# Kernel optimization log

Hardware: AMD Instinct MI355X
Metric: run time of the kernel (lower is better)

The kernel has to match this reference:

```python
import jax, jax.numpy as jnp
import numpy as np

N_NODES = 100000


def _gcn_conv(x, edge_index, W, b):
    """PyG GCNConv: add self-loops, symmetric deg^-1/2 normalization, scatter-add."""
    N = x.shape[0]
    h = x @ W  # [N, out]
    src = edge_index[0]
    dst = edge_index[1]
    loop = jnp.arange(N, dtype=src.dtype)
    src = jnp.concatenate([src, loop])
    dst = jnp.concatenate([dst, loop])
    deg = jax.ops.segment_sum(jnp.ones(src.shape[0], dtype=h.dtype), dst, num_segments=N)
    dinv = jnp.where(deg > 0, jax.lax.rsqrt(deg), 0.0)
    norm = dinv[src] * dinv[dst]  # [E+N]
    msgs = h[src] * norm[:, None]  # gather + scale
    out = jax.ops.segment_sum(msgs, dst, num_segments=N)  # scatter-add
    return out + b


def setup_inputs() -> dict:
    key = jax.random.key(0)
    k1, k2, k3, k4 = jax.random.split(key, 4)
    F_IN, H = 512, 16
    x = jax.random.normal(k1, (N_NODES, F_IN), dtype=jnp.float32)
    edge_index = jax.random.randint(k2, (2, 3200000), 0, N_NODES, dtype=jnp.int64)
    # Glorot init like PyG GCNConv
    lim = np.sqrt(6.0 / (F_IN + H)).astype(np.float32)
    W1 = jax.random.uniform(k3, (F_IN, H), dtype=jnp.float32, minval=-lim, maxval=lim)
    b1 = jnp.zeros((H,), dtype=jnp.float32)
    return {"x": x, "edge_index": edge_index, "W1": W1, "b1": b1}


def reference(x, edge_index, W1, b1):
    # forward: relu(GCNConv(x)); dropout is identity in eval; log_softmax over features
    h = jax.nn.relu(_gcn_conv(x, edge_index, W1, b1))
    return jax.nn.log_softmax(h, axis=1)
```

## Files before the change

### kernel.cpp

```cpp
#include <hip/hip_runtime.h>
#include <hip/hip_bf16.h>
#include <stdint.h>

#define N_NODES 100000
#define F_IN    512
#define HOUT    16

#define BSH   8
#define NBUK  391
#define CAP   9216
#define CHUNK 8192
#define GEMM_BLOCKS 782

typedef __attribute__((ext_vector_type(8))) short bf16x8;
typedef __attribute__((ext_vector_type(4))) float f32x4;

__device__ __forceinline__ short f2bf(float f) {
    union { float f; uint32_t u; } v; v.f = f;
    uint32_t r = (v.u + 0x7FFFu + ((v.u >> 16) & 1u)) >> 16;
    return (short)r;
}
__device__ __forceinline__ float bf2f(uint32_t bits16) {
    union { uint32_t u; float f; } v; v.u = bits16 << 16;
    return v.f;
}

__device__ __forceinline__ int edge_at(const void* ei, int64_t idx, uint32_t is64) {
    if (is64) return (int)((const long long*)ei)[idx];
    return ((const int*)ei)[idx];
}

__global__ void k_init(const uint32_t* __restrict__ e_u32, uint32_t* __restrict__ flag,
                       uint32_t* __restrict__ bucket_woff) {
    const int t = threadIdx.x;
    if (t < NBUK) bucket_woff[t] = 0u;
    if (t == 0) {
        uint32_t o = 0;
        #pragma unroll
        for (int i = 1; i < 32; i += 2) o |= e_u32[i];
        flag[0] = (o == 0u) ? 1u : 0u;
    }
}

__global__ __launch_bounds__(512) void k_fused(const void* __restrict__ ei, int E, int nchunks,
                                               const uint32_t* __restrict__ flag,
                                               uint32_t* __restrict__ bucket_woff,
                                               uint32_t* __restrict__ gpairs,
                                               const float* __restrict__ x,
                                               const float* __restrict__ W,
                                               ushort* __restrict__ hb) {
    __shared__ uint32_t h[512];
    __shared__ uint32_t ex[512];
    __shared__ uint32_t pcnt[512];
    __shared__ uint32_t gbase[512];
    __shared__ uint32_t sorted[CHUNK];
    __shared__ uint16_t sbuck[CHUNK];

    const int t = threadIdx.x;

    if ((int)blockIdx.x < nchunks) {
        const uint32_t is64 = flag[0];
        const int base = blockIdx.x * CHUNK;
        const int chunk_n = min(CHUNK, E - base);

        h[t] = 0;
        __syncthreads();

        uint32_t pr[16];
        uint16_t bk[16];
        #pragma unroll
        for (int k = 0; k < 16; ++k) {
            int e = base + k * 512 + t;
            bk[k] = 0xFFFFu;
            if (e < E) {
                uint32_t s = (uint32_t)edge_at(ei, e, is64);
                uint32_t d = (uint32_t)edge_at(ei, (int64_t)E + e, is64);
                uint32_t b = d >> BSH;
                pr[k] = (s << BSH) | (d & ((1u << BSH) - 1u));
                bk[k] = (uint16_t)b;
                atomicAdd(&h[b], 1u);
            }
        }
        __syncthreads();

        const uint32_t hv = h[t];
        for (int off = 1; off < 512; off <<= 1) {
            uint32_t v = (t >= off) ? h[t - off] : 0u;
            __syncthreads();
            h[t] += v;
            __syncthreads();
        }
        ex[t] = h[t] - hv;
        pcnt[t] = ex[t];
        if (t < NBUK) gbase[t] = atomicAdd(&bucket_woff[t], hv);
        __syncthreads();

        #pragma unroll
        for (int k = 0; k < 16; ++k) {
            if (bk[k] != 0xFFFFu) {
                uint32_t slot = atomicAdd(&pcnt[bk[k]], 1u);
                sorted[slot] = pr[k];
                sbuck[slot] = bk[k];
            }
        }
        __syncthreads();

        #pragma unroll
        for (int k = 0; k < 16; ++k) {
            int i = k * 512 + t;
            if (i < chunk_n) {
                uint32_t b = sbuck[i];
                uint32_t pos = gbase[b] + ((uint32_t)i - ex[b]);
                gpairs[(size_t)b * CAP + pos] = sorted[i];
            }
        }
    } else {
        const int lane = t & 63;
        const int wid  = t >> 6;
        const int tile = ((int)blockIdx.x - nchunks) * 8 + wid;
        if (tile * 16 >= N_NODES) return;
        const int c    = lane & 15;
        const int half = lane >> 4;

        bf16x8 bfrag[16];
        #pragma unroll
        for (int s = 0; s < 16; ++s) {
            #pragma unroll
            for (int e = 0; e < 8; ++e) {
                int k = 32 * s + 8 * half + e;
                bfrag[s][e] = f2bf(W[k * HOUT + c]);
            }
        }

        const int row = tile * 16 + c;
        const float* xr = x + (int64_t)row * F_IN;
        f32x4 acc = {0.f, 0.f, 0.f, 0.f};
        #pragma unroll
        for (int s = 0; s < 16; ++s) {
            const float4 a0 = *(const float4*)(xr + 32 * s + 8 * half);
            const float4 a1 = *(const float4*)(xr + 32 * s + 8 * half + 4);
            bf16x8 af;
            af[0] = f2bf(a0.x); af[1] = f2bf(a0.y); af[2] = f2bf(a0.z); af[3] = f2bf(a0.w);
            af[4] = f2bf(a1.x); af[5] = f2bf(a1.y); af[6] = f2bf(a1.z); af[7] = f2bf(a1.w);
            acc = __builtin_amdgcn_mfma_f32_16x16x32_bf16(af, bfrag[s], acc, 0, 0, 0);
        }

        #pragma unroll
        for (int r = 0; r < 4; ++r) {
            int orow = tile * 16 + 4 * half + r;
            hb[(int64_t)orow * HOUT + c] = (ushort)f2bf(acc[r]);
        }
    }
}

__global__ __launch_bounds__(256) void k_hist(const uint32_t* __restrict__ bucket_woff,
                                              const uint32_t* __restrict__ gpairs,
                                              uint32_t* __restrict__ cnt,
                                              ushort* __restrict__ hb) {
    const int b = blockIdx.x;
    const int t = threadIdx.x;
    const uint32_t count = bucket_woff[b];
    const uint32_t* gp = gpairs + (size_t)b * CAP;

    __shared__ uint32_t lc[256];
    lc[t] = 0;
    __syncthreads();
    for (uint32_t i = t; i < count; i += 256)
        atomicAdd(&lc[gp[i] & 255u], 1u);
    __syncthreads();

    const int gn = (b << BSH) + t;
    if (gn < N_NODES) {
        const uint32_t deg = lc[t];
        cnt[gn] = deg;
        const float dinv = rsqrtf((float)(deg + 1u));
        ushort* row = hb + (size_t)gn * HOUT;
        ulonglong4 rv = *(const ulonglong4*)row;
        ushort u[16];
        *(ulonglong4*)u = rv;
        #pragma unroll
        for (int q = 0; q < 16; ++q)
            u[q] = (ushort)f2bf(bf2f(u[q]) * dinv);
        *(ulonglong4*)row = *(const ulonglong4*)u;
    }
}

__global__ __launch_bounds__(1024) void k_sortagg(const uint32_t* __restrict__ bucket_woff,
                                                  const uint32_t* __restrict__ gpairs,
                                                  const uint32_t* __restrict__ cnt,
                                                  const ushort* __restrict__ hb,
                                                  const float* __restrict__ bias,
                                                  float* __restrict__ out) {
    const int bk = blockIdx.x;
    const int t = threadIdx.x;
    const uint32_t count = bucket_woff[bk];
    const uint32_t* gp = gpairs + (size_t)bk * CAP;

    __shared__ uint32_t lc[256];
    __shared__ uint32_t st[256];
    __shared__ uint32_t cur[256];
    __shared__ uint32_t sc[256];
    __shared__ uint32_t lsrc[CAP];

    if (t < 256) {
        int gn = (bk << BSH) + t;
        lc[t] = (gn < N_NODES) ? cnt[gn] : 0u;
        sc[t] = lc[t];
    }
    __syncthreads();
    for (int off = 1; off < 256; off <<= 1) {
        uint32_t v = 0;
        if (t < 256 && t >= off) v = sc[t - off];
        __syncthreads();
        if (t < 256) sc[t] += v;
        __syncthreads();
    }
    if (t < 256) {
        st[t] = sc[t] - lc[t];
        cur[t] = st[t];
    }
    __syncthreads();

    for (uint32_t i = t; i < count; i += 1024) {
        uint32_t p = gp[i];
        uint32_t pos = atomicAdd(&cur[p & 255u], 1u);
        lsrc[pos] = p >> BSH;
    }
    __syncthreads();

    const int f = t & 15;
    const int g = t >> 4;
    const float bf = bias[f];

    #pragma unroll
    for (int i = 0; i < 4; ++i) {
        int dl = g + 64 * i;
        int gn = (bk << BSH) + dl;
        if (gn >= N_NODES) break;
        const uint32_t s0 = st[dl];
        const uint32_t n  = lc[dl];

        float acc = 0.f;
        uint32_t j = 0;
        for (; j + 4 <= n; j += 4) {
            uint32_t a = lsrc[s0 + j], b2 = lsrc[s0 + j + 1];
            uint32_t c2 = lsrc[s0 + j + 2], d2 = lsrc[s0 + j + 3];
            float v0 = bf2f(hb[(size_t)a  * HOUT + f]);
            float v1 = bf2f(hb[(size_t)b2 * HOUT + f]);
            float v2 = bf2f(hb[(size_t)c2 * HOUT + f]);
            float v3 = bf2f(hb[(size_t)d2 * HOUT + f]);
            acc += (v0 + v1) + (v2 + v3);
        }
        for (; j < n; ++j)
            acc += bf2f(hb[(size_t)lsrc[s0 + j] * HOUT + f]);

        const float dinv = rsqrtf((float)(n + 1u));
        const float self = bf2f(hb[(size_t)gn * HOUT + f]);
        float v = fmaxf(fmaf(dinv, acc + self, bf), 0.f);

        float m = v;
        #pragma unroll
        for (int d = 1; d < 16; d <<= 1) m = fmaxf(m, __shfl_xor(m, d));
        float ex = __expf(v - m);
        float sum = ex;
        #pragma unroll
        for (int d = 1; d < 16; d <<= 1) sum += __shfl_xor(sum, d);
        out[(size_t)gn * HOUT + f] = v - (m + __logf(sum));
    }
}

extern "C" void kernel_launch(void* const* d_in, const int* in_sizes, int n_in,
                              void* d_out, int out_size, void* d_ws, size_t ws_size,
                              hipStream_t stream) {
    const float* x  = (const float*)d_in[0];
    const void*  ei = d_in[1];
    const float* W  = (const float*)d_in[2];
    const float* b  = (const float*)d_in[3];
    float* out = (float*)d_out;
    const int E = in_sizes[1] / 2;
    const int nchunks = (E + CHUNK - 1) / CHUNK;

    char* ws = (char*)d_ws;
    uint32_t* flag        = (uint32_t*)ws;
    uint32_t* bucket_woff = (uint32_t*)(ws + 1024);
    uint32_t* gpairs      = (uint32_t*)(ws + (1 << 20));
    ushort*   hb          = (ushort*)(ws + (16 << 20));
    uint32_t* cnt         = (uint32_t*)(ws + (20 << 20));

    k_init<<<1, 512, 0, stream>>>((const uint32_t*)ei, flag, bucket_woff);
    k_fused<<<nchunks + GEMM_BLOCKS, 512, 0, stream>>>(ei, E, nchunks, flag,
                                                       bucket_woff, gpairs, x, W, hb);
    k_hist<<<NBUK, 256, 0, stream>>>(bucket_woff, gpairs, cnt, hb);
    k_sortagg<<<NBUK, 1024, 0, stream>>>(bucket_woff, gpairs, cnt, hb, b, out);
}
```

Baseline: 105.0 us.

## Halve sort chunk, vectorize edge loads, wave-shuffle scans, paired-feature gather

Halves the bucket-sort chunk size so twice as many blocks share the edge partitioning, and loads two edges per thread with vector loads. The shared-memory Hillis-Steele scans in both kernels become wave-level shuffle scans plus a per-wave prefix, removing most block barriers. The aggregation kernel now has each thread gather two bf16 features with one 32-bit load and write float2 outputs, with the softmax reduction over 8 lanes. Smaller chunks mean more global atomics on bucket offsets, and the scan change relies on 64-wide wavefronts.

```diff
diff --git a/kernel.cpp b/kernel.cpp
--- a/kernel.cpp
+++ b/kernel.cpp
@@ -9,7 +9,7 @@
 #define BSH   8
 #define NBUK  391
 #define CAP   9216
-#define CHUNK 8192
+#define CHUNK 4096
 #define GEMM_BLOCKS 782
 
 typedef __attribute__((ext_vector_type(8))) short bf16x8;
@@ -62,41 +62,72 @@
         const uint32_t is64 = flag[0];
         const int base = blockIdx.x * CHUNK;
         const int chunk_n = min(CHUNK, E - base);
+        const bool evenE = ((E & 1) == 0);
 
         h[t] = 0;
         __syncthreads();
 
-        uint32_t pr[16];
-        uint16_t bk[16];
-        #pragma unroll
-        for (int k = 0; k < 16; ++k) {
-            int e = base + k * 512 + t;
-            bk[k] = 0xFFFFu;
-            if (e < E) {
-                uint32_t s = (uint32_t)edge_at(ei, e, is64);
-                uint32_t d = (uint32_t)edge_at(ei, (int64_t)E + e, is64);
-                uint32_t b = d >> BSH;
-                pr[k] = (s << BSH) | (d & ((1u << BSH) - 1u));
-                bk[k] = (uint16_t)b;
+        uint32_t pr[8];
+        uint16_t bk[8];
+        #pragma unroll
+        for (int k = 0; k < 4; ++k) {
+            const int e0 = base + k * 1024 + 2 * t;
+            uint32_t s0 = 0, s1 = 0, d0 = 0, d1 = 0;
+            const bool ok0 = (e0 < E), ok1 = (e0 + 1 < E);
+            if (ok1 && evenE) {
+                if (is64) {
+                    ulonglong2 S = *(const ulonglong2*)((const long long*)ei + e0);
+                    ulonglong2 D = *(const ulonglong2*)((const long long*)ei + (int64_t)E + e0);
+                    s0 = (uint32_t)S.x; s1 = (uint32_t)S.y;
+                    d0 = (uint32_t)D.x; d1 = (uint32_t)D.y;
+                } else {
+                    uint2 S = *(const uint2*)((const int*)ei + e0);
+                    uint2 D = *(const uint2*)((const int*)ei + (int64_t)E + e0);
+                    s0 = S.x; s1 = S.y; d0 = D.x; d1 = D.y;
+                }
+            } else {
+                if (ok0) { s0 = (uint32_t)edge_at(ei, e0, is64);
+                           d0 = (uint32_t)edge_at(ei, (int64_t)E + e0, is64); }
+                if (ok1) { s1 = (uint32_t)edge_at(ei, e0 + 1, is64);
+                           d1 = (uint32_t)edge_at(ei, (int64_t)E + e0 + 1, is64); }
+            }
+            bk[2*k]   = 0xFFFFu;
+            bk[2*k+1] = 0xFFFFu;
+            if (ok0) {
+                uint32_t b = d0 >> BSH;
+                pr[2*k] = (s0 << BSH) | (d0 & 255u);
+                bk[2*k] = (uint16_t)b;
                 atomicAdd(&h[b], 1u);
             }
+            if (ok1) {
+                uint32_t b = d1 >> BSH;
+                pr[2*k+1] = (s1 << BSH) | (d1 & 255u);
+                bk[2*k+1] = (uint16_t)b;
+                atomicAdd(&h[b], 1u);
+            }
         }
         __syncthreads();
 
         const uint32_t hv = h[t];
-        for (int off = 1; off < 512; off <<= 1) {
-            uint32_t v = (t >= off) ? h[t - off] : 0u;
-            __syncthreads();
-            h[t] += v;
-            __syncthreads();
-        }
-        ex[t] = h[t] - hv;
-        pcnt[t] = ex[t];
+        uint32_t v = hv;
+        #pragma unroll
+        for (int d = 1; d < 64; d <<= 1) {
+            uint32_t u = __shfl_up(v, d, 64);
+            if ((t & 63) >= d) v += u;
+        }
+        h[t] = v;
+        __syncthreads();
+        uint32_t wbase = 0;
+        const int w = t >> 6;
+        for (int w2 = 0; w2 < w; ++w2) wbase += h[w2 * 64 + 63];
+        const uint32_t exv = wbase + v - hv;
+        ex[t] = exv;
+        pcnt[t] = exv;
         if (t < NBUK) gbase[t] = atomicAdd(&bucket_woff[t], hv);
         __syncthreads();
 
         #pragma unroll
-        for (int k = 0; k < 16; ++k) {
+        for (int k = 0; k < 8; ++k) {
             if (bk[k] != 0xFFFFu) {
                 uint32_t slot = atomicAdd(&pcnt[bk[k]], 1u);
                 sorted[slot] = pr[k];
@@ -106,7 +137,7 @@
         __syncthreads();
 
         #pragma unroll
-        for (int k = 0; k < 16; ++k) {
+        for (int k = 0; k < 8; ++k) {
             int i = k * 512 + t;
             if (i < chunk_n) {
                 uint32_t b = sbuck[i];
@@ -195,30 +226,38 @@
     const int t = threadIdx.x;
     const uint32_t count = bucket_woff[bk];
     const uint32_t* gp = gpairs + (size_t)bk * CAP;
+    const uint32_t* hb32 = (const uint32_t*)hb;
 
     __shared__ uint32_t lc[256];
     __shared__ uint32_t st[256];
     __shared__ uint32_t cur[256];
-    __shared__ uint32_t sc[256];
     __shared__ uint32_t lsrc[CAP];
 
     if (t < 256) {
         int gn = (bk << BSH) + t;
         lc[t] = (gn < N_NODES) ? cnt[gn] : 0u;
-        sc[t] = lc[t];
-    }
-    __syncthreads();
-    for (int off = 1; off < 256; off <<= 1) {
-        uint32_t v = 0;
-        if (t < 256 && t >= off) v = sc[t - off];
-        __syncthreads();
-        if (t < 256) sc[t] += v;
-        __syncthreads();
-    }
+    }
+    __syncthreads();
     if (t < 256) {
-        st[t] = sc[t] - lc[t];
-        cur[t] = st[t];
-    }
+        const uint32_t hv = lc[t];
+        uint32_t v = hv;
+        #pragma unroll
+        for (int d = 1; d < 64; d <<= 1) {
+            uint32_t u = __shfl_up(v, d, 64);
+            if ((t & 63) >= d) v += u;
+        }
+        cur[t] = v;
+    }
+    __syncthreads();
+    if (t < 256) {
+        uint32_t wb = 0;
+        const int w = t >> 6;
+        for (int w2 = 0; w2 < w; ++w2) wb += cur[w2 * 64 + 63];
+        const uint32_t s = wb + cur[t] - lc[t];
+        st[t] = s;
+    }
+    __syncthreads();
+    if (t < 256) cur[t] = st[t];
     __syncthreads();
 
     for (uint32_t i = t; i < count; i += 1024) {
@@ -228,44 +267,54 @@
     }
     __syncthreads();
 
-    const int f = t & 15;
-    const int g = t >> 4;
-    const float bf = bias[f];
+    const int f8 = t & 7;
+    const int g  = t >> 3;
+    const float b0 = bias[2 * f8];
+    const float b1 = bias[2 * f8 + 1];
 
     #pragma unroll
-    for (int i = 0; i < 4; ++i) {
-        int dl = g + 64 * i;
+    for (int i = 0; i < 2; ++i) {
+        int dl = g + 128 * i;
         int gn = (bk << BSH) + dl;
         if (gn >= N_NODES) break;
         const uint32_t s0 = st[dl];
         const uint32_t n  = lc[dl];
 
-        float acc = 0.f;
+        float a0 = 0.f, a1 = 0.f;
         uint32_t j = 0;
         for (; j + 4 <= n; j += 4) {
-            uint32_t a = lsrc[s0 + j], b2 = lsrc[s0 + j + 1];
-            uint32_t c2 = lsrc[s0 + j + 2], d2 = lsrc[s0 + j + 3];
-            float v0 = bf2f(hb[(size_t)a  * HOUT + f]);
-            float v1 = bf2f(hb[(size_t)b2 * HOUT + f]);
-            float v2 = bf2f(hb[(size_t)c2 * HOUT + f]);
-            float v3 = bf2f(hb[(size_t)d2 * HOUT + f]);
-            acc += (v0 + v1) + (v2 + v3);
-        }
-        for (; j < n; ++j)
-            acc += bf2f(hb[(size_t)lsrc[s0 + j] * HOUT + f]);
+            uint32_t sA = lsrc[s0 + j],     sB = lsrc[s0 + j + 1];
+            uint32_t sC = lsrc[s0 + j + 2], sD = lsrc[s0 + j + 3];
+            uint32_t uA = hb32[(size_t)sA * 8 + f8];
+            uint32_t uB = hb32[(size_t)sB * 8 + f8];
+            uint32_t uC = hb32[(size_t)sC * 8 + f8];
+            uint32_t uD = hb32[(size_t)sD * 8 + f8];
+            a0 += (bf2f(uA & 0xFFFFu) + bf2f(uB & 0xFFFFu))
+                + (bf2f(uC & 0xFFFFu) + bf2f(uD & 0xFFFFu));
+            a1 += (bf2f(uA >> 16) + bf2f(uB >> 16))
+                + (bf2f(uC >> 16) + bf2f(uD >> 16));
+        }
+        for (; j < n; ++j) {
+            uint32_t u = hb32[(size_t)lsrc[s0 + j] * 8 + f8];
+            a0 += bf2f(u & 0xFFFFu);
+            a1 += bf2f(u >> 16);
+        }
 
         const float dinv = rsqrtf((float)(n + 1u));
-        const float self = bf2f(hb[(size_t)gn * HOUT + f]);
-        float v = fmaxf(fmaf(dinv, acc + self, bf), 0.f);
-
-        float m = v;
-        #pragma unroll
-        for (int d = 1; d < 16; d <<= 1) m = fmaxf(m, __shfl_xor(m, d));
-        float ex = __expf(v - m);
-        float sum = ex;
-        #pragma unroll
-        for (int d = 1; d < 16; d <<= 1) sum += __shfl_xor(sum, d);
-        out[(size_t)gn * HOUT + f] = v - (m + __logf(sum));
+        const uint32_t us = hb32[(size_t)gn * 8 + f8];
+        float v0 = fmaxf(fmaf(dinv, a0 + bf2f(us & 0xFFFFu), b0), 0.f);
+        float v1 = fmaxf(fmaf(dinv, a1 + bf2f(us >> 16), b1), 0.f);
+
+        float m = fmaxf(v0, v1);
+        #pragma unroll
+        for (int d = 1; d < 8; d <<= 1) m = fmaxf(m, __shfl_xor(m, d, 8));
+        float sum = __expf(v0 - m) + __expf(v1 - m);
+        #pragma unroll
+        for (int d = 1; d < 8; d <<= 1) sum += __shfl_xor(sum, d, 8);
+        const float ls = m + __logf(sum);
+
+        float2 o; o.x = v0 - ls; o.y = v1 - ls;
+        ((float2*)out)[(size_t)gn * 8 + f8] = o;
     }
 }
 
```

After: 108.3 us. 1.03x slower.
